# Performance work log

Measured on AMD Instinct MI355X. Metric: run time of the kernel, lower is better.

Reference implementation:

```python
import jax, jax.numpy as jnp
import numpy as np

N_NODES = 100000
N_EDGES = 1600000
HIDDEN = 128
OUT_DIM = 1
N_GRAPHS = 2048
VOCAB = 28  # atom types, Embedding(28, hidden_dim)


def setup_inputs() -> dict:
    key = jax.random.key(0)
    ks = jax.random.split(key, 14)
    s = 1.0 / np.sqrt(HIDDEN)
    inp = {
        "x_idx": jax.random.randint(ks[0], (N_NODES,), 0, VOCAB, dtype=jnp.int32),
        "edge_src": jax.random.randint(ks[1], (N_EDGES,), 0, N_NODES, dtype=jnp.int32),
        "edge_dst": jax.random.randint(ks[2], (N_EDGES,), 0, N_NODES, dtype=jnp.int32),
        "batch": jnp.sort(jax.random.randint(ks[3], (N_NODES,), 0, N_GRAPHS, dtype=jnp.int32)),
        # parameters
        "embed": jax.random.normal(ks[4], (VOCAB, HIDDEN), dtype=jnp.float32) * 0.02,
        "eps0": jnp.zeros((1,), dtype=jnp.float32),
        "w1_0": jax.random.normal(ks[5], (HIDDEN, HIDDEN), dtype=jnp.float32) * s,
        "b1_0": jnp.zeros((HIDDEN,), dtype=jnp.float32),
        "w2_0": jax.random.normal(ks[6], (HIDDEN, HIDDEN), dtype=jnp.float32) * s,
        "b2_0": jnp.zeros((HIDDEN,), dtype=jnp.float32),
        "eps1": jnp.zeros((1,), dtype=jnp.float32),
        "w1_1": jax.random.normal(ks[7], (HIDDEN, HIDDEN), dtype=jnp.float32) * s,
        "b1_1": jnp.zeros((HIDDEN,), dtype=jnp.float32),
        "w2_1": jax.random.normal(ks[8], (HIDDEN, OUT_DIM), dtype=jnp.float32) * s,
        "b2_1": jnp.zeros((OUT_DIM,), dtype=jnp.float32),
    }
    return inp


def _gin_layer(x, edge_src, edge_dst, eps, w1, b1, w2, b2):
    # A @ x via edge-list SpMM: out[dst] += x[src]  (same math as to_dense().matmul(x))
    agg = jax.ops.segment_sum(x[edge_src], edge_dst, num_segments=N_NODES)
    h = agg + (1.0 + eps) * x  # [N, in_feats]; eps broadcasts (shape [1])
    h = h @ w1 + b1            # linear1 (no nonlinearity between, as in source)
    return h @ w2 + b2         # linear2


def reference(x_idx, edge_src, edge_dst, batch, embed,
              eps0, w1_0, b1_0, w2_0, b2_0,
              eps1, w1_1, b1_1, w2_1, b2_1):
    x = embed[x_idx]  # [N, HIDDEN] — Embedding lookup (.squeeze(1) trivial here)
    x = jax.nn.relu(_gin_layer(x, edge_src, edge_dst, eps0, w1_0, b1_0, w2_0, b2_0))
    x = _gin_layer(x, edge_src, edge_dst, eps1, w1_1, b1_1, w2_1, b2_1)  # [N, 1]
    y_hat = jax.ops.segment_sum(x.squeeze(-1), batch, num_segments=N_GRAPHS)  # [G]
    return (y_hat, x)
```

## Files before the change

kernel.cpp:

```cpp
#include <hip/hip_runtime.h>

#define N_NODES  100000
#define N_EDGES  1600000
#define HIDDEN   128
#define N_GRAPHS 2048
#define VOCAB    28
#define NB       196
#define CAP      10000
#define EPB      6250
#define EPT      25
#define EWP      132
#define CSTR     29

__global__ void k_init(float* __restrict__ out, int* __restrict__ gcursor) {
    int i = blockIdx.x * blockDim.x + threadIdx.x;
    if (i < N_GRAPHS) out[i] = 0.0f;
    else if (i < N_GRAPHS + 256) gcursor[i - N_GRAPHS] = 0;
}

__global__ __launch_bounds__(256) void k_prep(const float* __restrict__ w1_0,
                                              const float* __restrict__ w2_0,
                                              const float* __restrict__ b1_0,
                                              const float* __restrict__ b2_0,
                                              const float* __restrict__ w1_1,
                                              const float* __restrict__ b1_1,
                                              const float* __restrict__ w2_1,
                                              const float* __restrict__ b2_1,
                                              float* __restrict__ Wc0,
                                              float* __restrict__ bc0,
                                              float* __restrict__ wc1,
                                              float* __restrict__ bc1) {
    int t = threadIdx.x;
    if (blockIdx.x < 64) {
        int g = blockIdx.x * 256 + t;
        int i = g >> 7, j = g & 127;
        float s = 0.f;
#pragma unroll 8
        for (int k = 0; k < HIDDEN; ++k)
            s += w1_0[i * HIDDEN + k] * w2_0[k * HIDDEN + j];
        Wc0[g] = s;
    } else {
        if (t < 128) {
            float s = 0.f;
#pragma unroll 8
            for (int k = 0; k < HIDDEN; ++k)
                s += b1_0[k] * w2_0[k * HIDDEN + t];
            bc0[t] = s + b2_0[t];
            if (t == 0) {
                float q = 0.f;
                for (int k = 0; k < HIDDEN; ++k) q += b1_1[k] * w2_1[k];
                bc1[0] = q + b2_1[0];
            }
        } else {
            int i = t - 128;
            float s = 0.f;
#pragma unroll 8
            for (int k = 0; k < HIDDEN; ++k)
                s += w1_1[i * HIDDEN + k] * w2_1[k];
            wc1[i] = s;
        }
    }
}

__global__ __launch_bounds__(256) void k_prep2(const float* __restrict__ embed,
                                               const float* __restrict__ Wc0,
                                               float* __restrict__ EW) {
    int g = blockIdx.x * 256 + threadIdx.x;
    if (g >= VOCAB * HIDDEN) return;
    int i = g >> 7, j = g & 127;
    float s = 0.f;
#pragma unroll 8
    for (int k = 0; k < HIDDEN; ++k)
        s += embed[i * HIDDEN + k] * Wc0[k * HIDDEN + j];
    EW[g] = s;
}

__global__ __launch_bounds__(256) void k_bin(const int* __restrict__ esrc,
                                             const int* __restrict__ edst,
                                             const int* __restrict__ x_idx,
                                             unsigned* __restrict__ binned,
                                             int* __restrict__ gcursor) {
    __shared__ int hist[256];
    __shared__ int scanbuf[256];
    __shared__ int lbase[256];
    __shared__ int lcur[256];
    __shared__ int gbase[256];
    __shared__ unsigned stage[EPB];
    __shared__ int tgt[EPB];

    const int tid = threadIdx.x;
    hist[tid] = 0;
    lcur[tid] = 0;
    __syncthreads();

    unsigned mypk[EPT];
    short    myb[EPT];
#pragma unroll
    for (int i = 0; i < EPT; ++i) {
        int idx = i * 256 + tid;
        myb[i] = -1;
        if (idx < EPB) {
            int e   = blockIdx.x * EPB + idx;
            int dst = edst[e];
            int src = esrc[e];
            int b   = dst >> 9;
            int dl  = dst & 511;
            int vix = x_idx[src];
            mypk[i] = ((unsigned)dl << 22) | ((unsigned)vix << 17) | (unsigned)src;
            myb[i]  = (short)b;
            atomicAdd(&hist[b], 1);
        }
    }
    __syncthreads();

    int v = hist[tid];
    scanbuf[tid] = v;
    __syncthreads();
    for (int off = 1; off < 256; off <<= 1) {
        int x = (tid >= off) ? scanbuf[tid - off] : 0;
        __syncthreads();
        scanbuf[tid] += x;
        __syncthreads();
    }
    lbase[tid] = scanbuf[tid] - v;
    if (tid < NB) gbase[tid] = (v > 0) ? atomicAdd(&gcursor[tid], v) : 0;
    __syncthreads();

#pragma unroll
    for (int i = 0; i < EPT; ++i) {
        if (myb[i] >= 0) {
            int b   = myb[i];
            int pos = lbase[b] + atomicAdd(&lcur[b], 1);
            stage[pos] = mypk[i];
            tgt[pos]   = b * CAP + gbase[b] + (pos - lbase[b]);
        }
    }
    __syncthreads();

    for (int i = tid; i < EPB; i += 256)
        binned[tgt[i]] = stage[i];
}

__global__ __launch_bounds__(256) void k_layerA(const unsigned* __restrict__ binned,
                                                const int* __restrict__ gcursor,
                                                const int* __restrict__ x_idx,
                                                const float* __restrict__ EW,
                                                const float* __restrict__ bc0,
                                                const float* __restrict__ wc1,
                                                const float* __restrict__ eps0,
                                                float* __restrict__ d) {
    __shared__ __align__(16) float ewp[VOCAB * EWP];
    __shared__ int lcnt[256 * CSTR];

    const int tid = threadIdx.x;
    const int b   = blockIdx.x >> 1;
    const int h   = blockIdx.x & 1;

    for (int i = tid; i < VOCAB * HIDDEN; i += 256) {
        int v = i >> 7, f = i & 127;
        ewp[v * EWP + f] = EW[i];
    }
    for (int i = tid; i < 256 * CSTR; i += 256) lcnt[i] = 0;
    __syncthreads();

    const int cnt = gcursor[b];
    const unsigned* bp = binned + (size_t)b * CAP;
    for (int i = tid; i < cnt; i += 256) {
        unsigned pk = bp[i];
        int dl = pk >> 22;
        if ((dl >> 8) == h)
            atomicAdd(&lcnt[(dl & 255) * CSTR + ((pk >> 17) & 31)], 1);
    }
    __syncthreads();

    const int nl = tid;
    const int n  = b * 512 + h * 256 + nl;

    float cf[VOCAB];
#pragma unroll
    for (int v = 0; v < VOCAB; ++v) cf[v] = (float)lcnt[nl * CSTR + v];

    const float s  = 1.0f + eps0[0];
    const int   xi = (n < N_NODES) ? x_idx[n] : 0;
    const float* exr = &ewp[xi * EWP];

    const float4* EW4 = reinterpret_cast<const float4*>(EW);
    const float4* b04 = reinterpret_cast<const float4*>(bc0);
    const float4* w14 = reinterpret_cast<const float4*>(wc1);

    float dacc = 0.f;
#pragma unroll 1
    for (int f4 = 0; f4 < 32; ++f4) {
        float4 a = b04[f4];
        float4 ex = *reinterpret_cast<const float4*>(exr + f4 * 4);
        a.x += s * ex.x; a.y += s * ex.y; a.z += s * ex.z; a.w += s * ex.w;
#pragma unroll
        for (int v = 0; v < VOCAB; ++v) {
            float4 e = EW4[v * 32 + f4];
            a.x += cf[v] * e.x;
            a.y += cf[v] * e.y;
            a.z += cf[v] * e.z;
            a.w += cf[v] * e.w;
        }
        float4 w = w14[f4];
        dacc += fmaxf(a.x, 0.f) * w.x + fmaxf(a.y, 0.f) * w.y
              + fmaxf(a.z, 0.f) * w.z + fmaxf(a.w, 0.f) * w.w;
    }
    if (n < N_NODES) d[n] = dacc;
}

__global__ __launch_bounds__(512) void k_B2(const unsigned* __restrict__ binned,
                                            const int* __restrict__ gcursor,
                                            const float* __restrict__ d,
                                            const int* __restrict__ batch,
                                            const float* __restrict__ eps1,
                                            const float* __restrict__ bc1,
                                            float* __restrict__ out) {
    __shared__ float racc[512];
    __shared__ float gacc[N_GRAPHS];

    const int tid = threadIdx.x;
    const int b   = blockIdx.x;
    const int n0  = b * 512;
    const int nlast = min(n0 + 511, N_NODES - 1);

    racc[tid] = 0.f;
    const int g0 = batch[n0];
    const int g1 = batch[nlast];
    for (int g = g0 + tid; g <= g1; g += 512) gacc[g] = 0.f;
    __syncthreads();

    const int cnt = gcursor[b];
    const unsigned* bp = binned + (size_t)b * CAP;
    for (int i = tid; i < cnt; i += 512) {
        unsigned pk = bp[i];
        atomicAdd(&racc[pk >> 22], d[pk & 0x1FFFFu]);
    }
    __syncthreads();

    int n = n0 + tid;
    if (n < N_NODES) {
        float r = (1.0f + eps1[0]) * d[n] + racc[tid] + bc1[0];
        out[N_GRAPHS + n] = r;
        atomicAdd(&gacc[batch[n]], r);
    }
    __syncthreads();
    for (int g = g0 + tid; g <= g1; g += 512) {
        float v = gacc[g];
        if (v != 0.f) atomicAdd(&out[g], v);
    }
}

extern "C" void kernel_launch(void* const* d_in, const int* in_sizes, int n_in,
                              void* d_out, int out_size, void* d_ws, size_t ws_size,
                              hipStream_t stream) {
    const int*   x_idx = (const int*)d_in[0];
    const int*   esrc  = (const int*)d_in[1];
    const int*   edst  = (const int*)d_in[2];
    const int*   batch = (const int*)d_in[3];
    const float* embed = (const float*)d_in[4];
    const float* eps0  = (const float*)d_in[5];
    const float* w1_0  = (const float*)d_in[6];
    const float* b1_0  = (const float*)d_in[7];
    const float* w2_0  = (const float*)d_in[8];
    const float* b2_0  = (const float*)d_in[9];
    const float* eps1  = (const float*)d_in[10];
    const float* w1_1  = (const float*)d_in[11];
    const float* b1_1  = (const float*)d_in[12];
    const float* w2_1  = (const float*)d_in[13];
    const float* b2_1  = (const float*)d_in[14];

    float* out = (float*)d_out;

    int*      gcursor = (int*)d_ws;
    unsigned* binned  = (unsigned*)(gcursor + 256);
    float*    d       = (float*)(binned + (size_t)NB * CAP);
    float*    Wc0     = d + N_NODES;
    float*    bc0     = Wc0 + HIDDEN * HIDDEN;
    float*    wc1     = bc0 + HIDDEN;
    float*    bc1     = wc1 + HIDDEN;
    float*    EW      = bc1 + 1;

    k_init<<<9, 256, 0, stream>>>(out, gcursor);

    k_prep<<<65, 256, 0, stream>>>(w1_0, w2_0, b1_0, b2_0, w1_1, b1_1, w2_1, b2_1,
                                   Wc0, bc0, wc1, bc1);
    k_prep2<<<(VOCAB * HIDDEN + 255) / 256, 256, 0, stream>>>(embed, Wc0, EW);

    k_bin<<<256, 256, 0, stream>>>(esrc, edst, x_idx, binned, gcursor);

    k_layerA<<<NB * 2, 256, 0, stream>>>(binned, gcursor, x_idx, EW, bc0, wc1, eps0, d);

    k_B2<<<NB, 512, 0, stream>>>(binned, gcursor, d, batch, eps1, bc1, out);
}
```

Before: 174.7 us.

## Fuse weight prep into binning kernel and restructure layerA compute per wave

The separate prep kernels are folded into an extra block of the binning kernel. That block computes EW as embed@w1_0@w2_0, reassociated so it never builds the full 128x128 Wc0 product, and the init kernel becomes memsets. In layerA, the self-term is folded into the float count row. Each wave now holds EW columns in registers per lane and loops over 64 nodes, reducing with shuffles, instead of each thread streaming EW float4s from global memory. This cuts launches and redundant global/LDS traffic. The cost is a serial extra block in binprep and 64 shuffle reductions per wave.

Result: slower. 231.9 us (+32.8%).

```diff
diff --git a/kernel.cpp b/kernel.cpp
--- a/kernel.cpp
+++ b/kernel.cpp
@@ -9,77 +9,26 @@
 #define CAP      10000
 #define EPB      6250
 #define EPT      25
-#define EWP      132
-#define CSTR     29
-
-__global__ void k_init(float* __restrict__ out, int* __restrict__ gcursor) {
-    int i = blockIdx.x * blockDim.x + threadIdx.x;
-    if (i < N_GRAPHS) out[i] = 0.0f;
-    else if (i < N_GRAPHS + 256) gcursor[i - N_GRAPHS] = 0;
-}
-
-__global__ __launch_bounds__(256) void k_prep(const float* __restrict__ w1_0,
-                                              const float* __restrict__ w2_0,
-                                              const float* __restrict__ b1_0,
-                                              const float* __restrict__ b2_0,
-                                              const float* __restrict__ w1_1,
-                                              const float* __restrict__ b1_1,
-                                              const float* __restrict__ w2_1,
-                                              const float* __restrict__ b2_1,
-                                              float* __restrict__ Wc0,
-                                              float* __restrict__ bc0,
-                                              float* __restrict__ wc1,
-                                              float* __restrict__ bc1) {
-    int t = threadIdx.x;
-    if (blockIdx.x < 64) {
-        int g = blockIdx.x * 256 + t;
-        int i = g >> 7, j = g & 127;
-        float s = 0.f;
-#pragma unroll 8
-        for (int k = 0; k < HIDDEN; ++k)
-            s += w1_0[i * HIDDEN + k] * w2_0[k * HIDDEN + j];
-        Wc0[g] = s;
-    } else {
-        if (t < 128) {
-            float s = 0.f;
-#pragma unroll 8
-            for (int k = 0; k < HIDDEN; ++k)
-                s += b1_0[k] * w2_0[k * HIDDEN + t];
-            bc0[t] = s + b2_0[t];
-            if (t == 0) {
-                float q = 0.f;
-                for (int k = 0; k < HIDDEN; ++k) q += b1_1[k] * w2_1[k];
-                bc1[0] = q + b2_1[0];
-            }
-        } else {
-            int i = t - 128;
-            float s = 0.f;
-#pragma unroll 8
-            for (int k = 0; k < HIDDEN; ++k)
-                s += w1_1[i * HIDDEN + k] * w2_1[k];
-            wc1[i] = s;
-        }
-    }
-}
-
-__global__ __launch_bounds__(256) void k_prep2(const float* __restrict__ embed,
-                                               const float* __restrict__ Wc0,
-                                               float* __restrict__ EW) {
-    int g = blockIdx.x * 256 + threadIdx.x;
-    if (g >= VOCAB * HIDDEN) return;
-    int i = g >> 7, j = g & 127;
-    float s = 0.f;
-#pragma unroll 8
-    for (int k = 0; k < HIDDEN; ++k)
-        s += embed[i * HIDDEN + k] * Wc0[k * HIDDEN + j];
-    EW[g] = s;
-}
-
-__global__ __launch_bounds__(256) void k_bin(const int* __restrict__ esrc,
-                                             const int* __restrict__ edst,
-                                             const int* __restrict__ x_idx,
-                                             unsigned* __restrict__ binned,
-                                             int* __restrict__ gcursor) {
+#define CSTR     32
+
+__global__ __launch_bounds__(256) void k_binprep(const int* __restrict__ esrc,
+                                                 const int* __restrict__ edst,
+                                                 const int* __restrict__ x_idx,
+                                                 unsigned* __restrict__ binned,
+                                                 int* __restrict__ gcursor,
+                                                 const float* __restrict__ embed,
+                                                 const float* __restrict__ w1_0,
+                                                 const float* __restrict__ b1_0,
+                                                 const float* __restrict__ w2_0,
+                                                 const float* __restrict__ b2_0,
+                                                 const float* __restrict__ w1_1,
+                                                 const float* __restrict__ b1_1,
+                                                 const float* __restrict__ w2_1,
+                                                 const float* __restrict__ b2_1,
+                                                 float* __restrict__ EW,
+                                                 float* __restrict__ bc0,
+                                                 float* __restrict__ wc1,
+                                                 float* __restrict__ bc1) {
     __shared__ int hist[256];
     __shared__ int scanbuf[256];
     __shared__ int lbase[256];
@@ -89,6 +38,48 @@
     __shared__ int tgt[EPB];
 
     const int tid = threadIdx.x;
+
+    if (blockIdx.x == 256) {
+        float* T = (float*)stage;
+        for (int o = tid; o < VOCAB * HIDDEN; o += 256) {
+            int i = o >> 7, j = o & 127;
+            float s = 0.f;
+#pragma unroll 8
+            for (int k = 0; k < HIDDEN; ++k)
+                s += embed[i * HIDDEN + k] * w1_0[k * HIDDEN + j];
+            T[o] = s;
+        }
+        __syncthreads();
+        for (int o = tid; o < VOCAB * HIDDEN; o += 256) {
+            int i = o >> 7, j = o & 127;
+            float s = 0.f;
+#pragma unroll 8
+            for (int k = 0; k < HIDDEN; ++k)
+                s += T[i * HIDDEN + k] * w2_0[k * HIDDEN + j];
+            EW[o] = s;
+        }
+        if (tid < 128) {
+            float s = 0.f;
+#pragma unroll 8
+            for (int k = 0; k < HIDDEN; ++k)
+                s += b1_0[k] * w2_0[k * HIDDEN + tid];
+            bc0[tid] = s + b2_0[tid];
+            if (tid == 0) {
+                float q = 0.f;
+                for (int k = 0; k < HIDDEN; ++k) q += b1_1[k] * w2_1[k];
+                bc1[0] = q + b2_1[0];
+            }
+        } else {
+            int i = tid - 128;
+            float s = 0.f;
+#pragma unroll 8
+            for (int k = 0; k < HIDDEN; ++k)
+                s += w1_1[i * HIDDEN + k] * w2_1[k];
+            wc1[i] = s;
+        }
+        return;
+    }
+
     hist[tid] = 0;
     lcur[tid] = 0;
     __syncthreads();
@@ -149,18 +140,13 @@
                                                 const float* __restrict__ wc1,
                                                 const float* __restrict__ eps0,
                                                 float* __restrict__ d) {
-    __shared__ __align__(16) float ewp[VOCAB * EWP];
-    __shared__ int lcnt[256 * CSTR];
+    __shared__ __align__(16) float lcnt[256 * CSTR];
 
     const int tid = threadIdx.x;
     const int b   = blockIdx.x >> 1;
     const int h   = blockIdx.x & 1;
 
-    for (int i = tid; i < VOCAB * HIDDEN; i += 256) {
-        int v = i >> 7, f = i & 127;
-        ewp[v * EWP + f] = EW[i];
-    }
-    for (int i = tid; i < 256 * CSTR; i += 256) lcnt[i] = 0;
+    for (int i = tid; i < 256 * CSTR; i += 256) lcnt[i] = 0.f;
     __syncthreads();
 
     const int cnt = gcursor[b];
@@ -169,44 +155,50 @@
         unsigned pk = bp[i];
         int dl = pk >> 22;
         if ((dl >> 8) == h)
-            atomicAdd(&lcnt[(dl & 255) * CSTR + ((pk >> 17) & 31)], 1);
-    }
-    __syncthreads();
-
-    const int nl = tid;
-    const int n  = b * 512 + h * 256 + nl;
-
-    float cf[VOCAB];
-#pragma unroll
-    for (int v = 0; v < VOCAB; ++v) cf[v] = (float)lcnt[nl * CSTR + v];
-
-    const float s  = 1.0f + eps0[0];
-    const int   xi = (n < N_NODES) ? x_idx[n] : 0;
-    const float* exr = &ewp[xi * EWP];
-
-    const float4* EW4 = reinterpret_cast<const float4*>(EW);
-    const float4* b04 = reinterpret_cast<const float4*>(bc0);
-    const float4* w14 = reinterpret_cast<const float4*>(wc1);
-
-    float dacc = 0.f;
+            atomicAdd(&lcnt[(dl & 255) * CSTR + ((pk >> 17) & 31)], 1.0f);
+    }
+    __syncthreads();
+
+    const int n_self = b * 512 + h * 256 + tid;
+    if (n_self < N_NODES)
+        lcnt[tid * CSTR + x_idx[n_self]] += 1.0f + eps0[0];
+    __syncthreads();
+
+    const int wave = tid >> 6, lane = tid & 63;
+
+    float ew0[VOCAB], ew1[VOCAB];
+#pragma unroll
+    for (int v = 0; v < VOCAB; ++v) {
+        ew0[v] = EW[v * HIDDEN + lane];
+        ew1[v] = EW[v * HIDDEN + lane + 64];
+    }
+    const float blo = bc0[lane], bhi = bc0[lane + 64];
+    const float wlo = wc1[lane], whi = wc1[lane + 64];
+
+    const int nbl = wave * 64;
+    float dmine = 0.f;
 #pragma unroll 1
-    for (int f4 = 0; f4 < 32; ++f4) {
-        float4 a = b04[f4];
-        float4 ex = *reinterpret_cast<const float4*>(exr + f4 * 4);
-        a.x += s * ex.x; a.y += s * ex.y; a.z += s * ex.z; a.w += s * ex.w;
-#pragma unroll
-        for (int v = 0; v < VOCAB; ++v) {
-            float4 e = EW4[v * 32 + f4];
-            a.x += cf[v] * e.x;
-            a.y += cf[v] * e.y;
-            a.z += cf[v] * e.z;
-            a.w += cf[v] * e.w;
-        }
-        float4 w = w14[f4];
-        dacc += fmaxf(a.x, 0.f) * w.x + fmaxf(a.y, 0.f) * w.y
-              + fmaxf(a.z, 0.f) * w.z + fmaxf(a.w, 0.f) * w.w;
-    }
-    if (n < N_NODES) d[n] = dacc;
+    for (int j = 0; j < 64; ++j) {
+        const float4* cp = reinterpret_cast<const float4*>(&lcnt[(nbl + j) * CSTR]);
+        float4 c0 = cp[0], c1 = cp[1], c2 = cp[2], c3 = cp[3];
+        float4 c4 = cp[4], c5 = cp[5], c6 = cp[6];
+        float a0 = blo, a1 = bhi;
+#define FM(cc, v) a0 = fmaf(cc, ew0[v], a0); a1 = fmaf(cc, ew1[v], a1);
+        FM(c0.x, 0)  FM(c0.y, 1)  FM(c0.z, 2)  FM(c0.w, 3)
+        FM(c1.x, 4)  FM(c1.y, 5)  FM(c1.z, 6)  FM(c1.w, 7)
+        FM(c2.x, 8)  FM(c2.y, 9)  FM(c2.z, 10) FM(c2.w, 11)
+        FM(c3.x, 12) FM(c3.y, 13) FM(c3.z, 14) FM(c3.w, 15)
+        FM(c4.x, 16) FM(c4.y, 17) FM(c4.z, 18) FM(c4.w, 19)
+        FM(c5.x, 20) FM(c5.y, 21) FM(c5.z, 22) FM(c5.w, 23)
+        FM(c6.x, 24) FM(c6.y, 25) FM(c6.z, 26) FM(c6.w, 27)
+#undef FM
+        float t = fmaxf(a0, 0.f) * wlo + fmaxf(a1, 0.f) * whi;
+#pragma unroll
+        for (int off = 32; off >= 1; off >>= 1) t += __shfl_xor(t, off, 64);
+        if (lane == j) dmine = t;
+    }
+    const int n = b * 512 + h * 256 + nbl + lane;
+    if (n < N_NODES) d[n] = dmine;
 }
 
 __global__ __launch_bounds__(512) void k_B2(const unsigned* __restrict__ binned,
@@ -275,19 +267,18 @@
     int*      gcursor = (int*)d_ws;
     unsigned* binned  = (unsigned*)(gcursor + 256);
     float*    d       = (float*)(binned + (size_t)NB * CAP);
-    float*    Wc0     = d + N_NODES;
-    float*    bc0     = Wc0 + HIDDEN * HIDDEN;
+    float*    bc0     = d + N_NODES;
     float*    wc1     = bc0 + HIDDEN;
     float*    bc1     = wc1 + HIDDEN;
     float*    EW      = bc1 + 1;
 
-    k_init<<<9, 256, 0, stream>>>(out, gcursor);
-
-    k_prep<<<65, 256, 0, stream>>>(w1_0, w2_0, b1_0, b2_0, w1_1, b1_1, w2_1, b2_1,
-                                   Wc0, bc0, wc1, bc1);
-    k_prep2<<<(VOCAB * HIDDEN + 255) / 256, 256, 0, stream>>>(embed, Wc0, EW);
-
-    k_bin<<<256, 256, 0, stream>>>(esrc, edst, x_idx, binned, gcursor);
+    hipMemsetAsync(out, 0, N_GRAPHS * sizeof(float), stream);
+    hipMemsetAsync(gcursor, 0, 256 * sizeof(int), stream);
+
+    k_binprep<<<257, 256, 0, stream>>>(esrc, edst, x_idx, binned, gcursor,
+                                       embed, w1_0, b1_0, w2_0, b2_0,
+                                       w1_1, b1_1, w2_1, b2_1,
+                                       EW, bc0, wc1, bc1);
 
     k_layerA<<<NB * 2, 256, 0, stream>>>(binned, gcursor, x_idx, EW, bc0, wc1, eps0, d);
 
```
